# Optimization experiments

Measured on AMD Instinct MI355X. Metric: run time of the kernel, lower is better.

The kernel has to match this reference:

```python
import jax, jax.numpy as jnp
import numpy as np

B, D_MODEL, D_INNER, N_STATE, K = 128, 2048, 4096, 128, 4


def setup_inputs() -> dict:
    key = jax.random.key(0)
    ks = jax.random.split(key, 10)
    def n(k, shape, s=1.0):
        return jax.random.normal(k, shape, dtype=jnp.float32) * s
    return {
        "x_t": n(ks[0], (B, D_MODEL)),
        "conv_state": n(ks[1], (B, D_INNER, K - 1)),
        "ssm_state": n(ks[2], (B, N_STATE, D_INNER), 0.1),
        "W_in": n(ks[3], (2 * D_INNER, D_MODEL), 0.02),
        "b_in": jnp.zeros((2 * D_INNER,), jnp.float32),
        "conv_weight": n(ks[4], (D_INNER, K), 0.1),
        # A = -exp(A_log) is always negative; sample in (-1, 0) for stability
        "A": -jax.random.uniform(ks[5], (N_STATE, D_INNER), dtype=jnp.float32),
        "B_param": n(ks[6], (N_STATE,), 0.1),
        "C_param": n(ks[7], (N_STATE,), 0.1),
        "D_param": jnp.ones((D_INNER,), jnp.float32),
        "W_out": n(ks[8], (D_MODEL, D_INNER), 0.02),
        "b_out": jnp.zeros((D_MODEL,), jnp.float32),
    }


def reference(x_t, conv_state, ssm_state, W_in, b_in, conv_weight, A,
              B_param, C_param, D_param, W_out, b_out):
    # in_proj, keep first d_inner channels (as in forward())
    x_proj = (x_t @ W_in.T + b_in)[:, :D_INNER]                      # (B, Di)
    # rolling causal conv update: window = [old K-1 samples, new sample]
    window = jnp.concatenate([conv_state, x_proj[:, :, None]], axis=-1)  # (B, Di, K)
    u = jax.nn.silu(jnp.sum(window * conv_weight[None], axis=-1))    # (B, Di)
    new_conv_state = window[:, :, 1:]                                 # (B, Di, K-1)
    # discretized SSM recurrence: h' = exp(A)*h + B u ; y = C.h + D u
    dA = jnp.exp(A)                                                   # (N, Di), in (e^-1, 1)
    new_ssm_state = dA[None] * ssm_state + B_param[None, :, None] * u[:, None, :]  # (B, N, Di)
    y_inner = jnp.einsum('n,bnd->bd', C_param, new_ssm_state) + D_param * u         # (B, Di)
    # out_proj back to d_model
    y_t = y_inner @ W_out.T + b_out                                   # (B, D)
    return (y_t, new_conv_state, new_ssm_state)
```

## Files before the change

### kernel.cpp

```cpp
#include <hip/hip_runtime.h>
#include <hip/hip_bf16.h>

#define DI 4096
#define DM 2048
#define NS 128
#define BB 128

typedef __attribute__((ext_vector_type(8))) short bf16x8;
typedef __attribute__((ext_vector_type(4))) float f32x4;

__device__ __forceinline__ unsigned short f2bf(float f) {
  union { __hip_bfloat16 h; unsigned short u; } c;
  c.h = __float2bfloat16(f);
  return c.u;
}

template<int N, int K, int NSPLIT>
__global__ __launch_bounds__(256) void gemm_bf16(
    const float* __restrict__ Xg, const float* __restrict__ Wg,
    float* __restrict__ part) {
  constexpr int NBLKS = N / 32;
  constexpr int KS = K / NSPLIT;
  constexpr int NSTEPS = KS / 32;
  const int nblk = blockIdx.x % NBLKS;
  const int ks   = blockIdx.x / NBLKS;
  const int kbase = ks * KS;
  const int tid = threadIdx.x;
  const int lane = tid & 63;
  const int wid = tid >> 6;
  const int wr = wid & 1;
  const int wc = wid >> 1;
  const int r16 = lane & 15;
  const int kb = lane >> 4;

  __shared__ __hip_bfloat16 As[128][40];
  __shared__ __hip_bfloat16 Bs[32][40];

  const int arow = tid >> 3;
  const int seg  = tid & 7;

  f32x4 acc[4] = { {0,0,0,0}, {0,0,0,0}, {0,0,0,0}, {0,0,0,0} };

  const float* aG = Xg + (size_t)arow * K + kbase + seg * 4;
  const float* bG = Wg + (size_t)(nblk * 32 + arow) * K + kbase + seg * 4;

  float4 pa0 = *(const float4*)(aG + 0 * 32 * K);
  float4 pa1 = *(const float4*)(aG + 1 * 32 * K);
  float4 pa2 = *(const float4*)(aG + 2 * 32 * K);
  float4 pa3 = *(const float4*)(aG + 3 * 32 * K);
  float4 pb  = *(const float4*)(bG);

  for (int step = 0; step < NSTEPS; ++step) {
    if (step) __syncthreads();
    {
      ushort4 h;
      h.x = f2bf(pa0.x); h.y = f2bf(pa0.y); h.z = f2bf(pa0.z); h.w = f2bf(pa0.w);
      *(ushort4*)&As[arow +  0][seg * 4] = h;
      h.x = f2bf(pa1.x); h.y = f2bf(pa1.y); h.z = f2bf(pa1.z); h.w = f2bf(pa1.w);
      *(ushort4*)&As[arow + 32][seg * 4] = h;
      h.x = f2bf(pa2.x); h.y = f2bf(pa2.y); h.z = f2bf(pa2.z); h.w = f2bf(pa2.w);
      *(ushort4*)&As[arow + 64][seg * 4] = h;
      h.x = f2bf(pa3.x); h.y = f2bf(pa3.y); h.z = f2bf(pa3.z); h.w = f2bf(pa3.w);
      *(ushort4*)&As[arow + 96][seg * 4] = h;
      h.x = f2bf(pb.x);  h.y = f2bf(pb.y);  h.z = f2bf(pb.z);  h.w = f2bf(pb.w);
      *(ushort4*)&Bs[arow][seg * 4] = h;
    }
    if (step + 1 < NSTEPS) {
      const float* aN = aG + (step + 1) * 32;
      pa0 = *(const float4*)(aN + 0 * 32 * K);
      pa1 = *(const float4*)(aN + 1 * 32 * K);
      pa2 = *(const float4*)(aN + 2 * 32 * K);
      pa3 = *(const float4*)(aN + 3 * 32 * K);
      pb  = *(const float4*)(bG + (step + 1) * 32);
    }
    __syncthreads();
    bf16x8 bv = *(const bf16x8*)&Bs[wc * 16 + r16][kb * 8];
#pragma unroll
    for (int m = 0; m < 4; ++m) {
      bf16x8 av = *(const bf16x8*)&As[wr * 64 + m * 16 + r16][kb * 8];
      acc[m] = __builtin_amdgcn_mfma_f32_16x16x32_bf16(av, bv, acc[m], 0, 0, 0);
    }
  }

  const int ncol = nblk * 32 + wc * 16 + r16;
#pragma unroll
  for (int m = 0; m < 4; ++m) {
#pragma unroll
    for (int r = 0; r < 4; ++r) {
      int brow = wr * 64 + m * 16 + kb * 4 + r;
      part[(size_t)(ks * 128 + brow) * N + ncol] = acc[m][r];
    }
  }
}

__global__ __launch_bounds__(256) void combine1(
    const float* __restrict__ part, const float* __restrict__ b_in,
    const float* __restrict__ conv_state, const float* __restrict__ conv_weight,
    float* __restrict__ u_ws, float* __restrict__ ncs) {
  int idx = blockIdx.x * 256 + threadIdx.x;
  int d = idx & (DI - 1);
  float xp = b_in[d];
#pragma unroll
  for (int s = 0; s < 4; ++s) xp += part[(size_t)s * (BB * DI) + idx];
  const float* cs = conv_state + (size_t)idx * 3;
  float4 w4 = *(const float4*)(conv_weight + d * 4);
  float c0 = cs[0], c1 = cs[1], c2 = cs[2];
  float sv = c0 * w4.x + c1 * w4.y + c2 * w4.z + xp * w4.w;
  float uu = sv / (1.f + __expf(-sv));
  u_ws[idx] = uu;
  float* o = ncs + (size_t)idx * 3;
  o[0] = c1; o[1] = c2; o[2] = xp;
}

__global__ __launch_bounds__(256) void ssm_kernel(
    const float* __restrict__ ssm, const float* __restrict__ A,
    const float* __restrict__ Bp, const float* __restrict__ Cp,
    const float* __restrict__ Dp, const float* __restrict__ u,
    float* __restrict__ nss, float* __restrict__ y_in) {
  const int chunk = blockIdx.x >> 7;
  const int b = blockIdx.x & 127;
  const int d0 = chunk * 1024 + threadIdx.x * 4;
  f32x4 u4  = *(const f32x4*)(u + (size_t)b * DI + d0);
  f32x4 dp4 = *(const f32x4*)(Dp + d0);
  float accx = dp4[0] * u4[0], accy = dp4[1] * u4[1];
  float accz = dp4[2] * u4[2], accw = dp4[3] * u4[3];
  const float* sp = ssm + (size_t)b * NS * DI + d0;
  float* op = nss + (size_t)b * NS * DI + d0;
#pragma unroll 4
  for (int n = 0; n < NS; ++n) {
    f32x4 a4 = *(const f32x4*)(A + (size_t)n * DI + d0);
    f32x4 s4 = __builtin_nontemporal_load((const f32x4*)(sp + (size_t)n * DI));
    float bn = Bp[n], cn = Cp[n];
    f32x4 ns4;
    ns4[0] = __expf(a4[0]) * s4[0] + bn * u4[0];
    ns4[1] = __expf(a4[1]) * s4[1] + bn * u4[1];
    ns4[2] = __expf(a4[2]) * s4[2] + bn * u4[2];
    ns4[3] = __expf(a4[3]) * s4[3] + bn * u4[3];
    __builtin_nontemporal_store(ns4, (f32x4*)(op + (size_t)n * DI));
    accx += cn * ns4[0]; accy += cn * ns4[1];
    accz += cn * ns4[2]; accw += cn * ns4[3];
  }
  f32x4 r; r[0] = accx; r[1] = accy; r[2] = accz; r[3] = accw;
  *(f32x4*)(y_in + (size_t)b * DI + d0) = r;
}

__global__ __launch_bounds__(256) void combine2(
    const float* __restrict__ part, const float* __restrict__ b_out,
    float* __restrict__ y_t) {
  int idx = blockIdx.x * 256 + threadIdx.x;
  int j = idx & (DM - 1);
  float v = b_out[j];
#pragma unroll
  for (int s = 0; s < 8; ++s) v += part[(size_t)s * (BB * DM) + idx];
  y_t[idx] = v;
}

extern "C" void kernel_launch(void* const* d_in, const int* in_sizes, int n_in,
                              void* d_out, int out_size, void* d_ws, size_t ws_size,
                              hipStream_t stream) {
  const float* x_t         = (const float*)d_in[0];
  const float* conv_state  = (const float*)d_in[1];
  const float* ssm_state   = (const float*)d_in[2];
  const float* W_in        = (const float*)d_in[3];
  const float* b_in        = (const float*)d_in[4];
  const float* conv_weight = (const float*)d_in[5];
  const float* A           = (const float*)d_in[6];
  const float* Bp          = (const float*)d_in[7];
  const float* Cp          = (const float*)d_in[8];
  const float* Dp          = (const float*)d_in[9];
  const float* W_out       = (const float*)d_in[10];
  const float* b_out       = (const float*)d_in[11];

  float* y_t = (float*)d_out;
  float* ncs = y_t + (size_t)BB * DM;
  float* nss = ncs + (size_t)BB * DI * 3;

  float* ws = (float*)d_ws;
  const size_t P1 = 4u * BB * DI;
  const size_t P2 = 8u * BB * DM;
  const size_t UV = (size_t)BB * DI;
  float *part1, *part2, *u_ws, *y_in;
  if (ws_size >= (P1 + P2 + 2 * UV) * sizeof(float)) {
    part1 = ws; part2 = part1 + P1; u_ws = part2 + P2; y_in = u_ws + UV;
  } else {
    part1 = nss;
    part2 = ws; u_ws = part2 + P2; y_in = u_ws + UV;
  }

  gemm_bf16<DI, DM, 4><<<dim3(512), dim3(256), 0, stream>>>(x_t, W_in, part1);
  combine1<<<dim3(2048), dim3(256), 0, stream>>>(part1, b_in, conv_state,
                                                 conv_weight, u_ws, ncs);
  ssm_kernel<<<dim3(512), dim3(256), 0, stream>>>(ssm_state, A, Bp, Cp, Dp,
                                                  u_ws, nss, y_in);
  gemm_bf16<DM, DI, 8><<<dim3(512), dim3(256), 0, stream>>>(y_in, W_out, part2);
  combine2<<<dim3(1024), dim3(256), 0, stream>>>(part2, b_out, y_t);
}
```

Measured before the change: 131.2 us.

## Fuse conv update into SSM kernel and double split-K factors for both GEMMs

The conv-window update, SiLU and reduction of the in_proj split-K partials are folded into the SSM kernel, which drops the separate combine1 launch and the round trip of u through memory. Conv state is now read and written as vectorized 16-byte loads and stores. Both GEMMs double their split-K factor (8 and 16), launching 1024 blocks each, which costs more partial-sum traffic for the reductions. The workspace is reused between part1 and part2, and the old path is kept as a fallback when the workspace is too small.

```diff
diff --git a/kernel.cpp b/kernel.cpp
--- a/kernel.cpp
+++ b/kernel.cpp
@@ -93,40 +93,62 @@
   }
 }
 
-__global__ __launch_bounds__(256) void combine1(
-    const float* __restrict__ part, const float* __restrict__ b_in,
+template<int NSPLIT>
+__global__ __launch_bounds__(256) void ssm_fused(
+    const float* __restrict__ part1, const float* __restrict__ b_in,
     const float* __restrict__ conv_state, const float* __restrict__ conv_weight,
-    float* __restrict__ u_ws, float* __restrict__ ncs) {
-  int idx = blockIdx.x * 256 + threadIdx.x;
-  int d = idx & (DI - 1);
-  float xp = b_in[d];
-#pragma unroll
-  for (int s = 0; s < 4; ++s) xp += part[(size_t)s * (BB * DI) + idx];
-  const float* cs = conv_state + (size_t)idx * 3;
-  float4 w4 = *(const float4*)(conv_weight + d * 4);
-  float c0 = cs[0], c1 = cs[1], c2 = cs[2];
-  float sv = c0 * w4.x + c1 * w4.y + c2 * w4.z + xp * w4.w;
-  float uu = sv / (1.f + __expf(-sv));
-  u_ws[idx] = uu;
-  float* o = ncs + (size_t)idx * 3;
-  o[0] = c1; o[1] = c2; o[2] = xp;
-}
-
-__global__ __launch_bounds__(256) void ssm_kernel(
     const float* __restrict__ ssm, const float* __restrict__ A,
     const float* __restrict__ Bp, const float* __restrict__ Cp,
-    const float* __restrict__ Dp, const float* __restrict__ u,
-    float* __restrict__ nss, float* __restrict__ y_in) {
+    const float* __restrict__ Dp,
+    float* __restrict__ ncs, float* __restrict__ nss, float* __restrict__ y_in) {
   const int chunk = blockIdx.x >> 7;
   const int b = blockIdx.x & 127;
   const int d0 = chunk * 1024 + threadIdx.x * 4;
-  f32x4 u4  = *(const f32x4*)(u + (size_t)b * DI + d0);
+  const size_t idx = (size_t)b * DI + d0;
+
+  f32x4 xp = *(const f32x4*)(b_in + d0);
+#pragma unroll
+  for (int s = 0; s < NSPLIT; ++s) {
+    f32x4 p = *(const f32x4*)(part1 + (size_t)s * (BB * DI) + idx);
+    xp[0] += p[0]; xp[1] += p[1]; xp[2] += p[2]; xp[3] += p[3];
+  }
+
+  const float* cs = conv_state + idx * 3;
+  f32x4 cv0 = __builtin_nontemporal_load((const f32x4*)(cs));
+  f32x4 cv1 = __builtin_nontemporal_load((const f32x4*)(cs + 4));
+  f32x4 cv2 = __builtin_nontemporal_load((const f32x4*)(cs + 8));
+  float4 w0 = *(const float4*)(conv_weight + (size_t)(d0 + 0) * 4);
+  float4 w1 = *(const float4*)(conv_weight + (size_t)(d0 + 1) * 4);
+  float4 w2 = *(const float4*)(conv_weight + (size_t)(d0 + 2) * 4);
+  float4 w3 = *(const float4*)(conv_weight + (size_t)(d0 + 3) * 4);
+
+  float sv0 = cv0[0]*w0.x + cv0[1]*w0.y + cv0[2]*w0.z + xp[0]*w0.w;
+  float sv1 = cv0[3]*w1.x + cv1[0]*w1.y + cv1[1]*w1.z + xp[1]*w1.w;
+  float sv2 = cv1[2]*w2.x + cv1[3]*w2.y + cv2[0]*w2.z + xp[2]*w2.w;
+  float sv3 = cv2[1]*w3.x + cv2[2]*w3.y + cv2[3]*w3.z + xp[3]*w3.w;
+
+  f32x4 u4;
+  u4[0] = sv0 / (1.f + __expf(-sv0));
+  u4[1] = sv1 / (1.f + __expf(-sv1));
+  u4[2] = sv2 / (1.f + __expf(-sv2));
+  u4[3] = sv3 / (1.f + __expf(-sv3));
+
+  f32x4 n0, n1, n2;
+  n0[0] = cv0[1]; n0[1] = cv0[2]; n0[2] = xp[0]; n0[3] = cv1[0];
+  n1[0] = cv1[1]; n1[1] = xp[1];  n1[2] = cv1[3]; n1[3] = cv2[0];
+  n2[0] = xp[2];  n2[1] = cv2[2]; n2[2] = cv2[3]; n2[3] = xp[3];
+  float* on = ncs + idx * 3;
+  __builtin_nontemporal_store(n0, (f32x4*)(on));
+  __builtin_nontemporal_store(n1, (f32x4*)(on + 4));
+  __builtin_nontemporal_store(n2, (f32x4*)(on + 8));
+
   f32x4 dp4 = *(const f32x4*)(Dp + d0);
-  float accx = dp4[0] * u4[0], accy = dp4[1] * u4[1];
-  float accz = dp4[2] * u4[2], accw = dp4[3] * u4[3];
+  float accx = dp4[0]*u4[0], accy = dp4[1]*u4[1];
+  float accz = dp4[2]*u4[2], accw = dp4[3]*u4[3];
+
   const float* sp = ssm + (size_t)b * NS * DI + d0;
   float* op = nss + (size_t)b * NS * DI + d0;
-#pragma unroll 4
+#pragma unroll 8
   for (int n = 0; n < NS; ++n) {
     f32x4 a4 = *(const f32x4*)(A + (size_t)n * DI + d0);
     f32x4 s4 = __builtin_nontemporal_load((const f32x4*)(sp + (size_t)n * DI));
@@ -141,9 +163,61 @@
     accz += cn * ns4[2]; accw += cn * ns4[3];
   }
   f32x4 r; r[0] = accx; r[1] = accy; r[2] = accz; r[3] = accw;
+  *(f32x4*)(y_in + idx) = r;
+}
+
+__global__ __launch_bounds__(256) void combine1(
+    const float* __restrict__ part, const float* __restrict__ b_in,
+    const float* __restrict__ conv_state, const float* __restrict__ conv_weight,
+    float* __restrict__ u_ws, float* __restrict__ ncs) {
+  int idx = blockIdx.x * 256 + threadIdx.x;
+  int d = idx & (DI - 1);
+  float xp = b_in[d];
+#pragma unroll
+  for (int s = 0; s < 4; ++s) xp += part[(size_t)s * (BB * DI) + idx];
+  const float* cs = conv_state + (size_t)idx * 3;
+  float4 w4 = *(const float4*)(conv_weight + d * 4);
+  float c0 = cs[0], c1 = cs[1], c2 = cs[2];
+  float sv = c0 * w4.x + c1 * w4.y + c2 * w4.z + xp * w4.w;
+  float uu = sv / (1.f + __expf(-sv));
+  u_ws[idx] = uu;
+  float* o = ncs + (size_t)idx * 3;
+  o[0] = c1; o[1] = c2; o[2] = xp;
+}
+
+__global__ __launch_bounds__(256) void ssm_kernel(
+    const float* __restrict__ ssm, const float* __restrict__ A,
+    const float* __restrict__ Bp, const float* __restrict__ Cp,
+    const float* __restrict__ Dp, const float* __restrict__ u,
+    float* __restrict__ nss, float* __restrict__ y_in) {
+  const int chunk = blockIdx.x >> 7;
+  const int b = blockIdx.x & 127;
+  const int d0 = chunk * 1024 + threadIdx.x * 4;
+  f32x4 u4  = *(const f32x4*)(u + (size_t)b * DI + d0);
+  f32x4 dp4 = *(const f32x4*)(Dp + d0);
+  float accx = dp4[0]*u4[0], accy = dp4[1]*u4[1];
+  float accz = dp4[2]*u4[2], accw = dp4[3]*u4[3];
+  const float* sp = ssm + (size_t)b * NS * DI + d0;
+  float* op = nss + (size_t)b * NS * DI + d0;
+#pragma unroll 8
+  for (int n = 0; n < NS; ++n) {
+    f32x4 a4 = *(const f32x4*)(A + (size_t)n * DI + d0);
+    f32x4 s4 = __builtin_nontemporal_load((const f32x4*)(sp + (size_t)n * DI));
+    float bn = Bp[n], cn = Cp[n];
+    f32x4 ns4;
+    ns4[0] = __expf(a4[0]) * s4[0] + bn * u4[0];
+    ns4[1] = __expf(a4[1]) * s4[1] + bn * u4[1];
+    ns4[2] = __expf(a4[2]) * s4[2] + bn * u4[2];
+    ns4[3] = __expf(a4[3]) * s4[3] + bn * u4[3];
+    __builtin_nontemporal_store(ns4, (f32x4*)(op + (size_t)n * DI));
+    accx += cn * ns4[0]; accy += cn * ns4[1];
+    accz += cn * ns4[2]; accw += cn * ns4[3];
+  }
+  f32x4 r; r[0] = accx; r[1] = accy; r[2] = accz; r[3] = accw;
   *(f32x4*)(y_in + (size_t)b * DI + d0) = r;
 }
 
+template<int NSPLIT>
 __global__ __launch_bounds__(256) void combine2(
     const float* __restrict__ part, const float* __restrict__ b_out,
     float* __restrict__ y_t) {
@@ -151,7 +225,7 @@
   int j = idx & (DM - 1);
   float v = b_out[j];
 #pragma unroll
-  for (int s = 0; s < 8; ++s) v += part[(size_t)s * (BB * DM) + idx];
+  for (int s = 0; s < NSPLIT; ++s) v += part[(size_t)s * (BB * DM) + idx];
   y_t[idx] = v;
 }
 
@@ -176,22 +250,34 @@
   float* nss = ncs + (size_t)BB * DI * 3;
 
   float* ws = (float*)d_ws;
-  const size_t P1 = 4u * BB * DI;
-  const size_t P2 = 8u * BB * DM;
-  const size_t UV = (size_t)BB * DI;
-  float *part1, *part2, *u_ws, *y_in;
-  if (ws_size >= (P1 + P2 + 2 * UV) * sizeof(float)) {
-    part1 = ws; part2 = part1 + P1; u_ws = part2 + P2; y_in = u_ws + UV;
+  const size_t P1F = 8u  * BB * DI;
+  const size_t P2F = 16u * BB * DM;
+  const size_t YV  = (size_t)BB * DI;
+
+  if (ws_size >= (P1F + YV) * sizeof(float)) {
+    float* part1 = ws;
+    float* part2 = ws;
+    float* y_in  = ws + (P1F > P2F ? P1F : P2F);
+
+    gemm_bf16<DI, DM, 8><<<dim3(1024), dim3(256), 0, stream>>>(x_t, W_in, part1);
+    ssm_fused<8><<<dim3(512), dim3(256), 0, stream>>>(
+        part1, b_in, conv_state, conv_weight, ssm_state, A, Bp, Cp, Dp,
+        ncs, nss, y_in);
+    gemm_bf16<DM, DI, 16><<<dim3(1024), dim3(256), 0, stream>>>(y_in, W_out, part2);
+    combine2<16><<<dim3(1024), dim3(256), 0, stream>>>(part2, b_out, y_t);
   } else {
-    part1 = nss;
-    part2 = ws; u_ws = part2 + P2; y_in = u_ws + UV;
-  }
-
-  gemm_bf16<DI, DM, 4><<<dim3(512), dim3(256), 0, stream>>>(x_t, W_in, part1);
-  combine1<<<dim3(2048), dim3(256), 0, stream>>>(part1, b_in, conv_state,
-                                                 conv_weight, u_ws, ncs);
-  ssm_kernel<<<dim3(512), dim3(256), 0, stream>>>(ssm_state, A, Bp, Cp, Dp,
-                                                  u_ws, nss, y_in);
-  gemm_bf16<DM, DI, 8><<<dim3(512), dim3(256), 0, stream>>>(y_in, W_out, part2);
-  combine2<<<dim3(1024), dim3(256), 0, stream>>>(part2, b_out, y_t);
-}
+    const size_t P2 = 8u * BB * DM;
+    float* part1 = nss;
+    float* part2 = ws;
+    float* u_ws  = part2 + P2;
+    float* y_in  = u_ws + YV;
+
+    gemm_bf16<DI, DM, 4><<<dim3(512), dim3(256), 0, stream>>>(x_t, W_in, part1);
+    combine1<<<dim3(2048), dim3(256), 0, stream>>>(part1, b_in, conv_state,
+                                                   conv_weight, u_ws, ncs);
+    ssm_kernel<<<dim3(512), dim3(256), 0, stream>>>(ssm_state, A, Bp, Cp, Dp,
+                                                    u_ws, nss, y_in);
+    gemm_bf16<DM, DI, 8><<<dim3(512), dim3(256), 0, stream>>>(y_in, W_out, part2);
+    combine2<8><<<dim3(1024), dim3(256), 0, stream>>>(part2, b_out, y_t);
+  }
+}
```

Measured after the change: 185.8 us. 41.6% more time.

## Double split-K in both GEMMs and split SSM state dimension across blocks

Applied to the files above, without the earlier changes.

Both projection GEMMs double their split-K factor (4→8, 8→16), launching 1024 blocks instead of 512 to fill more compute units. The SSM kernel splits the N_STATE loop into two halves, each writing a partial y_inner that the second GEMM sums on load through a new SUMX path. The cost is larger partial-sum buffers and more combine traffic, with a fallback to the old config when the workspace is small.

```diff
diff --git a/kernel.cpp b/kernel.cpp
--- a/kernel.cpp
+++ b/kernel.cpp
@@ -15,10 +15,20 @@
   return c.u;
 }
 
-template<int N, int K, int NSPLIT>
+template<bool SUMX>
+__device__ __forceinline__ float4 ldx(const float* p, const float* p2) {
+  float4 a = *(const float4*)p;
+  if constexpr (SUMX) {
+    float4 b = *(const float4*)p2;
+    a.x += b.x; a.y += b.y; a.z += b.z; a.w += b.w;
+  }
+  return a;
+}
+
+template<int N, int K, int NSPLIT, bool SUMX>
 __global__ __launch_bounds__(256) void gemm_bf16(
-    const float* __restrict__ Xg, const float* __restrict__ Wg,
-    float* __restrict__ part) {
+    const float* __restrict__ Xg, const float* __restrict__ Xg2,
+    const float* __restrict__ Wg, float* __restrict__ part) {
   constexpr int NBLKS = N / 32;
   constexpr int KS = K / NSPLIT;
   constexpr int NSTEPS = KS / 32;
@@ -41,13 +51,15 @@
 
   f32x4 acc[4] = { {0,0,0,0}, {0,0,0,0}, {0,0,0,0}, {0,0,0,0} };
 
-  const float* aG = Xg + (size_t)arow * K + kbase + seg * 4;
-  const float* bG = Wg + (size_t)(nblk * 32 + arow) * K + kbase + seg * 4;
-
-  float4 pa0 = *(const float4*)(aG + 0 * 32 * K);
-  float4 pa1 = *(const float4*)(aG + 1 * 32 * K);
-  float4 pa2 = *(const float4*)(aG + 2 * 32 * K);
-  float4 pa3 = *(const float4*)(aG + 3 * 32 * K);
+  const size_t aoff = (size_t)arow * K + kbase + seg * 4;
+  const float* aG  = Xg + aoff;
+  const float* aG2 = SUMX ? (Xg2 + aoff) : nullptr;
+  const float* bG  = Wg + (size_t)(nblk * 32 + arow) * K + kbase + seg * 4;
+
+  float4 pa0 = ldx<SUMX>(aG + 0 * 32 * K, SUMX ? aG2 + 0 * 32 * K : nullptr);
+  float4 pa1 = ldx<SUMX>(aG + 1 * 32 * K, SUMX ? aG2 + 1 * 32 * K : nullptr);
+  float4 pa2 = ldx<SUMX>(aG + 2 * 32 * K, SUMX ? aG2 + 2 * 32 * K : nullptr);
+  float4 pa3 = ldx<SUMX>(aG + 3 * 32 * K, SUMX ? aG2 + 3 * 32 * K : nullptr);
   float4 pb  = *(const float4*)(bG);
 
   for (int step = 0; step < NSTEPS; ++step) {
@@ -66,12 +78,12 @@
       *(ushort4*)&Bs[arow][seg * 4] = h;
     }
     if (step + 1 < NSTEPS) {
-      const float* aN = aG + (step + 1) * 32;
-      pa0 = *(const float4*)(aN + 0 * 32 * K);
-      pa1 = *(const float4*)(aN + 1 * 32 * K);
-      pa2 = *(const float4*)(aN + 2 * 32 * K);
-      pa3 = *(const float4*)(aN + 3 * 32 * K);
-      pb  = *(const float4*)(bG + (step + 1) * 32);
+      const int o = (step + 1) * 32;
+      pa0 = ldx<SUMX>(aG + o + 0 * 32 * K, SUMX ? aG2 + o + 0 * 32 * K : nullptr);
+      pa1 = ldx<SUMX>(aG + o + 1 * 32 * K, SUMX ? aG2 + o + 1 * 32 * K : nullptr);
+      pa2 = ldx<SUMX>(aG + o + 2 * 32 * K, SUMX ? aG2 + o + 2 * 32 * K : nullptr);
+      pa3 = ldx<SUMX>(aG + o + 3 * 32 * K, SUMX ? aG2 + o + 3 * 32 * K : nullptr);
+      pb  = *(const float4*)(bG + o);
     }
     __syncthreads();
     bf16x8 bv = *(const bf16x8*)&Bs[wc * 16 + r16][kb * 8];
@@ -93,6 +105,7 @@
   }
 }
 
+template<int NSPL>
 __global__ __launch_bounds__(256) void combine1(
     const float* __restrict__ part, const float* __restrict__ b_in,
     const float* __restrict__ conv_state, const float* __restrict__ conv_weight,
@@ -101,7 +114,7 @@
   int d = idx & (DI - 1);
   float xp = b_in[d];
 #pragma unroll
-  for (int s = 0; s < 4; ++s) xp += part[(size_t)s * (BB * DI) + idx];
+  for (int s = 0; s < NSPL; ++s) xp += part[(size_t)s * (BB * DI) + idx];
   const float* cs = conv_state + (size_t)idx * 3;
   float4 w4 = *(const float4*)(conv_weight + d * 4);
   float c0 = cs[0], c1 = cs[1], c2 = cs[2];
@@ -112,38 +125,48 @@
   o[0] = c1; o[1] = c2; o[2] = xp;
 }
 
+template<int NSP>
 __global__ __launch_bounds__(256) void ssm_kernel(
     const float* __restrict__ ssm, const float* __restrict__ A,
     const float* __restrict__ Bp, const float* __restrict__ Cp,
     const float* __restrict__ Dp, const float* __restrict__ u,
     float* __restrict__ nss, float* __restrict__ y_in) {
-  const int chunk = blockIdx.x >> 7;
+  constexpr int CNT = NS / NSP;
+  const int half  = blockIdx.x >> 9;
+  const int chunk = (blockIdx.x >> 7) & 3;
   const int b = blockIdx.x & 127;
+  const int n0 = half * CNT;
   const int d0 = chunk * 1024 + threadIdx.x * 4;
   f32x4 u4  = *(const f32x4*)(u + (size_t)b * DI + d0);
-  f32x4 dp4 = *(const f32x4*)(Dp + d0);
-  float accx = dp4[0] * u4[0], accy = dp4[1] * u4[1];
-  float accz = dp4[2] * u4[2], accw = dp4[3] * u4[3];
-  const float* sp = ssm + (size_t)b * NS * DI + d0;
-  float* op = nss + (size_t)b * NS * DI + d0;
+  float accx, accy, accz, accw;
+  if (half == 0) {
+    f32x4 dp4 = *(const f32x4*)(Dp + d0);
+    accx = dp4[0]*u4[0]; accy = dp4[1]*u4[1];
+    accz = dp4[2]*u4[2]; accw = dp4[3]*u4[3];
+  } else {
+    accx = accy = accz = accw = 0.f;
+  }
+  const float* sp = ssm + (size_t)b * NS * DI + (size_t)n0 * DI + d0;
+  float* op = nss + (size_t)b * NS * DI + (size_t)n0 * DI + d0;
 #pragma unroll 4
-  for (int n = 0; n < NS; ++n) {
-    f32x4 a4 = *(const f32x4*)(A + (size_t)n * DI + d0);
-    f32x4 s4 = __builtin_nontemporal_load((const f32x4*)(sp + (size_t)n * DI));
-    float bn = Bp[n], cn = Cp[n];
+  for (int i = 0; i < CNT; ++i) {
+    f32x4 a4 = *(const f32x4*)(A + (size_t)(n0 + i) * DI + d0);
+    f32x4 s4 = __builtin_nontemporal_load((const f32x4*)(sp + (size_t)i * DI));
+    float bn = Bp[n0 + i], cn = Cp[n0 + i];
     f32x4 ns4;
     ns4[0] = __expf(a4[0]) * s4[0] + bn * u4[0];
     ns4[1] = __expf(a4[1]) * s4[1] + bn * u4[1];
     ns4[2] = __expf(a4[2]) * s4[2] + bn * u4[2];
     ns4[3] = __expf(a4[3]) * s4[3] + bn * u4[3];
-    __builtin_nontemporal_store(ns4, (f32x4*)(op + (size_t)n * DI));
+    __builtin_nontemporal_store(ns4, (f32x4*)(op + (size_t)i * DI));
     accx += cn * ns4[0]; accy += cn * ns4[1];
     accz += cn * ns4[2]; accw += cn * ns4[3];
   }
   f32x4 r; r[0] = accx; r[1] = accy; r[2] = accz; r[3] = accw;
-  *(f32x4*)(y_in + (size_t)b * DI + d0) = r;
-}
-
+  *(f32x4*)(y_in + (size_t)half * (BB * DI) + (size_t)b * DI + d0) = r;
+}
+
+template<int NSPL>
 __global__ __launch_bounds__(256) void combine2(
     const float* __restrict__ part, const float* __restrict__ b_out,
     float* __restrict__ y_t) {
@@ -151,7 +174,7 @@
   int j = idx & (DM - 1);
   float v = b_out[j];
 #pragma unroll
-  for (int s = 0; s < 8; ++s) v += part[(size_t)s * (BB * DM) + idx];
+  for (int s = 0; s < NSPL; ++s) v += part[(size_t)s * (BB * DM) + idx];
   y_t[idx] = v;
 }
 
@@ -176,22 +199,53 @@
   float* nss = ncs + (size_t)BB * DI * 3;
 
   float* ws = (float*)d_ws;
-  const size_t P1 = 4u * BB * DI;
-  const size_t P2 = 8u * BB * DM;
-  const size_t UV = (size_t)BB * DI;
-  float *part1, *part2, *u_ws, *y_in;
-  if (ws_size >= (P1 + P2 + 2 * UV) * sizeof(float)) {
-    part1 = ws; part2 = part1 + P1; u_ws = part2 + P2; y_in = u_ws + UV;
+  const size_t UV  = (size_t)BB * DI;
+  const size_t P1  = 8u  * BB * DI;
+  const size_t P2  = 16u * BB * DM;
+  const size_t Y2  = 2 * UV;
+
+  if (ws_size >= (P1 + P2 + UV + Y2) * sizeof(float)) {
+    float* part1 = ws;
+    float* part2 = part1 + P1;
+    float* u_ws  = part2 + P2;
+    float* y_in  = u_ws + UV;
+    gemm_bf16<DI, DM, 8, false><<<dim3(1024), dim3(256), 0, stream>>>(
+        x_t, nullptr, W_in, part1);
+    combine1<8><<<dim3(2048), dim3(256), 0, stream>>>(
+        part1, b_in, conv_state, conv_weight, u_ws, ncs);
+    ssm_kernel<2><<<dim3(1024), dim3(256), 0, stream>>>(
+        ssm_state, A, Bp, Cp, Dp, u_ws, nss, y_in);
+    gemm_bf16<DM, DI, 16, true><<<dim3(1024), dim3(256), 0, stream>>>(
+        y_in, y_in + UV, W_out, part2);
+    combine2<16><<<dim3(1024), dim3(256), 0, stream>>>(part2, b_out, y_t);
+  } else if (ws_size >= (P2 + UV + Y2) * sizeof(float)) {
+    float* part1 = nss;
+    float* part2 = ws;
+    float* u_ws  = part2 + P2;
+    float* y_in  = u_ws + UV;
+    gemm_bf16<DI, DM, 8, false><<<dim3(1024), dim3(256), 0, stream>>>(
+        x_t, nullptr, W_in, part1);
+    combine1<8><<<dim3(2048), dim3(256), 0, stream>>>(
+        part1, b_in, conv_state, conv_weight, u_ws, ncs);
+    ssm_kernel<2><<<dim3(1024), dim3(256), 0, stream>>>(
+        ssm_state, A, Bp, Cp, Dp, u_ws, nss, y_in);
+    gemm_bf16<DM, DI, 16, true><<<dim3(1024), dim3(256), 0, stream>>>(
+        y_in, y_in + UV, W_out, part2);
+    combine2<16><<<dim3(1024), dim3(256), 0, stream>>>(part2, b_out, y_t);
   } else {
-    part1 = nss;
-    part2 = ws; u_ws = part2 + P2; y_in = u_ws + UV;
-  }
-
-  gemm_bf16<DI, DM, 4><<<dim3(512), dim3(256), 0, stream>>>(x_t, W_in, part1);
-  combine1<<<dim3(2048), dim3(256), 0, stream>>>(part1, b_in, conv_state,
-                                                 conv_weight, u_ws, ncs);
-  ssm_kernel<<<dim3(512), dim3(256), 0, stream>>>(ssm_state, A, Bp, Cp, Dp,
-                                                  u_ws, nss, y_in);
-  gemm_bf16<DM, DI, 8><<<dim3(512), dim3(256), 0, stream>>>(y_in, W_out, part2);
-  combine2<<<dim3(1024), dim3(256), 0, stream>>>(part2, b_out, y_t);
-}
+    const size_t P2s = 8u * BB * DM;
+    float* part1 = nss;
+    float* part2 = ws;
+    float* u_ws  = part2 + P2s;
+    float* y_in  = u_ws + UV;
+    gemm_bf16<DI, DM, 4, false><<<dim3(512), dim3(256), 0, stream>>>(
+        x_t, nullptr, W_in, part1);
+    combine1<4><<<dim3(2048), dim3(256), 0, stream>>>(
+        part1, b_in, conv_state, conv_weight, u_ws, ncs);
+    ssm_kernel<1><<<dim3(512), dim3(256), 0, stream>>>(
+        ssm_state, A, Bp, Cp, Dp, u_ws, nss, y_in);
+    gemm_bf16<DM, DI, 8, false><<<dim3(512), dim3(256), 0, stream>>>(
+        y_in, nullptr, W_out, part2);
+    combine2<8><<<dim3(1024), dim3(256), 0, stream>>>(part2, b_out, y_t);
+  }
+}
```

New measurement: 142.7 us. +8.8%, slower.
